# Kernel optimization log

Measured on AMD Instinct MI355X. Metric: run time of the kernel, lower is better.

Reference implementation:

```python
import jax, jax.numpy as jnp
import numpy as np

# Device / mapping constants (from iterator config in the original repo)
V_REF = 0.25
K_V = 2.0 * V_REF
G_MIN = 1e-5
G_MAX = 1e-3
N_AVG = 2.99
N_STD = 0.37
N_IN, N_OUT, BATCH = 1024, 512, 128


def setup_inputs() -> dict:
    key = jax.random.key(0)
    ks = jax.random.split(key, 6)
    x = jax.random.uniform(ks[0], (BATCH, N_IN), dtype=jnp.float32)
    stdv = 1.0 / np.sqrt(N_IN)
    w_pos = 0.5 + stdv * jax.random.normal(ks[1], (N_IN, N_OUT), dtype=jnp.float32)
    w_neg = 0.5 + stdv * jax.random.normal(ks[2], (N_IN, N_OUT), dtype=jnp.float32)
    b_pos = 0.5 * jnp.ones((N_OUT,), jnp.float32)
    b_neg = 0.5 * jnp.ones((N_OUT,), jnp.float32)
    # per-crosspoint I-V nonlinearity parameter n (n=2 means ohmic); clip below at 2
    n_devices = jnp.maximum(
        N_AVG + N_STD * jax.random.normal(ks[3], (N_IN + 1, 2 * N_OUT), dtype=jnp.float32),
        2.0,
    )
    return {"x": x, "w_pos": w_pos, "w_neg": w_neg, "b_pos": b_pos,
            "b_neg": b_neg, "n_devices": n_devices}


def reference(x, w_pos, w_neg, b_pos, b_neg, n_devices):
    B = x.shape[0]
    # append bias input of 1s -> [B, n_in+1]
    inputs = jnp.concatenate([x, jnp.ones((B, 1), x.dtype)], axis=1)
    # combined weights with bias row -> [n_in+1, n_out] each
    cw_pos = jnp.concatenate([w_pos, b_pos[None, :]], axis=0)
    cw_neg = jnp.concatenate([w_neg, b_neg[None, :]], axis=0)
    # interleave pos/neg columns -> [n_in+1, 2*n_out]
    combined = jnp.stack([cw_pos, cw_neg], axis=-1).reshape(cw_pos.shape[0], -1)
    # x -> V mapping
    V = K_V * inputs  # [B, n_in+1]
    # weight params -> conductances
    max_weight = jnp.max(jnp.abs(combined))
    k_G = (G_MAX - G_MIN) / max_weight
    G = k_G * jnp.abs(combined) + G_MIN  # [n_in+1, 2*n_out]
    # nonlinear I-V: I(V) = sign(V) * G*V_ref * (|V|/V_ref)^log2(n)
    exponent = jnp.log2(n_devices)          # [n_in+1, 2*n_out]
    sgn = jnp.sign(V)                       # [B, n_in+1]
    ratio = jnp.abs(V) / V_REF              # [B, n_in+1]
    I_ind = (sgn[:, :, None] * (G * V_REF)[None, :, :]
             * ratio[:, :, None] ** exponent[None, :, :])  # [B, n_in+1, 2*n_out]
    I = jnp.sum(I_ind, axis=1)              # [B, 2*n_out] (sum along bit lines)
    # differential pair currents -> output
    I_total = I[:, 0::2] - I[:, 1::2]       # [B, n_out]
    y = I_total / (K_V * k_G)
    return y
```

## Files before the change

kernel.cpp:

```cpp
#include <hip/hip_runtime.h>
#include <cstdint>
#include <cstddef>


#define B128 128
#define NIN  1024
#define NI   1025
#define NO   512
#define NJ   1024
#define SPLITS 32
#define CHUNK  33
#define GMIN 1.0e-5f
#define GSPAN (1.0e-3f - 1.0e-5f)

__device__ __forceinline__ float flog2(float x) { return __builtin_amdgcn_logf(x); }
__device__ __forceinline__ float fexp2(float x) { return __builtin_amdgcn_exp2f(x); }

__global__ __launch_bounds__(1024) void k_prep(
    const float* __restrict__ x,
    const float* __restrict__ wp, const float* __restrict__ wn,
    const float* __restrict__ bp, const float* __restrict__ bn,
    float* __restrict__ LT, float* __restrict__ bmax, float* __restrict__ out)
{
    const int tid = blockIdx.x * 1024 + threadIdx.x;

    if (tid < B128 * NO) out[tid] = 0.0f;

    if (tid < NI * B128) {
        int i = tid >> 7, b = tid & 127;
        float xv = (i < NIN) ? x[b * NIN + i] : 1.0f;
        LT[tid] = 1.0f + flog2(xv);
    }

    float m = fmaxf(fmaxf(__builtin_fabsf(wp[tid]), __builtin_fabsf(wn[tid])),
                    fmaxf(__builtin_fabsf(wp[tid + 262144]), __builtin_fabsf(wn[tid + 262144])));
    if (tid < NO) m = fmaxf(m, fmaxf(__builtin_fabsf(bp[tid]), __builtin_fabsf(bn[tid])));

    __shared__ float red[16];
    #pragma unroll
    for (int off = 32; off > 0; off >>= 1) m = fmaxf(m, __shfl_down(m, off, 64));
    if ((threadIdx.x & 63) == 0) red[threadIdx.x >> 6] = m;
    __syncthreads();
    if (threadIdx.x < 16) {
        m = red[threadIdx.x];
        #pragma unroll
        for (int off = 8; off > 0; off >>= 1) m = fmaxf(m, __shfl_down(m, off, 16));
        if (threadIdx.x == 0) bmax[blockIdx.x] = m;
    }
}

__global__ __launch_bounds__(1024, 4) void k_main(
    const float* __restrict__ nd,
    const float* __restrict__ wp, const float* __restrict__ wn,
    const float* __restrict__ bp, const float* __restrict__ bn,
    const float* __restrict__ LT, const float* __restrict__ bmax,
    float* __restrict__ out)
{
    const int lane = threadIdx.x & 63;

    float m = fmaxf(fmaxf(bmax[lane], bmax[lane + 64]),
                    fmaxf(bmax[lane + 128], bmax[lane + 192]));
    #pragma unroll
    for (int off = 32; off > 0; off >>= 1) m = fmaxf(m, __shfl_down(m, off, 64));
    const float maxw = __shfl(m, 0, 64);
    const float kG = GSPAN / maxw;
    const float C  = 0.5f * maxw / GSPAN;

    const int wvid = threadIdx.x >> 6;
    const int b0 = __builtin_amdgcn_readfirstlane(wvid << 3);
    const int o = (blockIdx.x << 6) + lane;
    const int i0 = blockIdx.y * CHUNK;
    int i1 = i0 + CHUNK; if (i1 > NI) i1 = NI;

    float2 acc[8];
    #pragma unroll
    for (int k = 0; k < 8; ++k) acc[k] = make_float2(0.0f, 0.0f);

    float2 nv = *(const float2*)(nd + (size_t)i0 * NJ + 2 * o);
    float wvp = (i0 < NIN) ? wp[i0 * NO + o] : bp[o];
    float wvn = (i0 < NIN) ? wn[i0 * NO + o] : bn[o];
    float4 L03 = *(const float4*)(LT + i0 * B128 + b0);
    float4 L47 = *(const float4*)(LT + i0 * B128 + b0 + 4);

    for (int i = i0; i < i1; ++i) {
        const int ip = (i + 1 < i1) ? i + 1 : i;
        float2 nv_n = *(const float2*)(nd + (size_t)ip * NJ + 2 * o);
        float wp_n = (ip < NIN) ? wp[ip * NO + o] : bp[o];
        float wn_n = (ip < NIN) ? wn[ip * NO + o] : bn[o];
        float4 L03n = *(const float4*)(LT + ip * B128 + b0);
        float4 L47n = *(const float4*)(LT + ip * B128 + b0 + 4);

        const float Ep = flog2(nv.x);
        const float En = flog2(nv.y);
        const float Wp = flog2(__builtin_fmaf(kG, __builtin_fabsf(wvp), GMIN));
        const float Wn = flog2(__builtin_fmaf(kG, __builtin_fabsf(wvn), GMIN));

        float Lv[8] = {L03.x, L03.y, L03.z, L03.w, L47.x, L47.y, L47.z, L47.w};
        #pragma unroll
        for (int bb = 0; bb < 8; ++bb) {
            const float L = Lv[bb];
            acc[bb].x += fexp2(__builtin_fmaf(Ep, L, Wp));
            acc[bb].y += fexp2(__builtin_fmaf(En, L, Wn));
        }

        nv = nv_n; wvp = wp_n; wvn = wn_n; L03 = L03n; L47 = L47n;
    }

    #pragma unroll
    for (int bb = 0; bb < 8; ++bb) {
        unsafeAtomicAdd(out + (size_t)(b0 + bb) * NO + o, C * (acc[bb].x - acc[bb].y));
    }
}

extern "C" void kernel_launch(void* const* d_in, const int* in_sizes, int n_in,
                              void* d_out, int out_size, void* d_ws, size_t ws_size,
                              hipStream_t stream)
{
    const float* x  = (const float*)d_in[0];
    const float* wp = (const float*)d_in[1];
    const float* wn = (const float*)d_in[2];
    const float* bp = (const float*)d_in[3];
    const float* bn = (const float*)d_in[4];
    const float* nd = (const float*)d_in[5];
    float* out = (float*)d_out;

    unsigned char* ws = (unsigned char*)d_ws;
    float* bmax = (float*)ws;
    float* LT   = (float*)(ws + 4096);

    k_prep<<<256, 1024, 0, stream>>>(x, wp, wn, bp, bn, LT, bmax, out);
    k_main<<<dim3(8, SPLITS), 1024, 0, stream>>>(nd, wp, wn, bp, bn, LT, bmax, out);
}
```

Before: 96.86 us.

## Precompute per-crosspoint log2 exponent and conductance in separate kernel

Adds a k_ew kernel that computes log2(n) and log2(G) for every crosspoint once and stores them as a float4 table. The main kernel then reads this table instead of recomputing four log2 per crosspoint in each of the 16 waves that share an output column. This removes redundant transcendental work, at the cost of an extra kernel launch and writing then reading an 8 MB intermediate table.

```diff
diff --git a/kernel.cpp b/kernel.cpp
--- a/kernel.cpp
+++ b/kernel.cpp
@@ -49,12 +49,43 @@
     }
 }
 
-__global__ __launch_bounds__(1024, 4) void k_main(
+__global__ __launch_bounds__(256) void k_ew(
     const float* __restrict__ nd,
     const float* __restrict__ wp, const float* __restrict__ wn,
     const float* __restrict__ bp, const float* __restrict__ bn,
-    const float* __restrict__ LT, const float* __restrict__ bmax,
-    float* __restrict__ out)
+    const float* __restrict__ bmax, float4* __restrict__ EWT)
+{
+    __shared__ float smax;
+    float m = bmax[threadIdx.x];
+    #pragma unroll
+    for (int off = 32; off > 0; off >>= 1) m = fmaxf(m, __shfl_down(m, off, 64));
+    __shared__ float red[4];
+    if ((threadIdx.x & 63) == 0) red[threadIdx.x >> 6] = m;
+    __syncthreads();
+    if (threadIdx.x == 0)
+        smax = fmaxf(fmaxf(red[0], red[1]), fmaxf(red[2], red[3]));
+    __syncthreads();
+    const float kG = GSPAN / smax;
+
+    const int tid = blockIdx.x * 256 + threadIdx.x;
+    if (tid >= NI * NO) return;
+    const int i = tid / NO, o = tid - i * NO;
+
+    const float2 nv = *(const float2*)(nd + (size_t)i * NJ + 2 * o);
+    const float wvp = (i < NIN) ? wp[i * NO + o] : bp[o];
+    const float wvn = (i < NIN) ? wn[i * NO + o] : bn[o];
+
+    float4 r;
+    r.x = flog2(nv.x);
+    r.y = flog2(__builtin_fmaf(kG, __builtin_fabsf(wvp), GMIN));
+    r.z = flog2(nv.y);
+    r.w = flog2(__builtin_fmaf(kG, __builtin_fabsf(wvn), GMIN));
+    EWT[tid] = r;
+}
+
+__global__ __launch_bounds__(1024, 4) void k_main(
+    const float4* __restrict__ EWT, const float* __restrict__ LT,
+    const float* __restrict__ bmax, float* __restrict__ out)
 {
     const int lane = threadIdx.x & 63;
 
@@ -63,52 +94,41 @@
     #pragma unroll
     for (int off = 32; off > 0; off >>= 1) m = fmaxf(m, __shfl_down(m, off, 64));
     const float maxw = __shfl(m, 0, 64);
-    const float kG = GSPAN / maxw;
     const float C  = 0.5f * maxw / GSPAN;
 
     const int wvid = threadIdx.x >> 6;
-    const int b0 = __builtin_amdgcn_readfirstlane(wvid << 3);
+    const int b0 = wvid << 3;
     const int o = (blockIdx.x << 6) + lane;
     const int i0 = blockIdx.y * CHUNK;
     int i1 = i0 + CHUNK; if (i1 > NI) i1 = NI;
 
-    float2 acc[8];
+    float accp[8], accn[8];
     #pragma unroll
-    for (int k = 0; k < 8; ++k) acc[k] = make_float2(0.0f, 0.0f);
+    for (int k = 0; k < 8; ++k) { accp[k] = 0.0f; accn[k] = 0.0f; }
 
-    float2 nv = *(const float2*)(nd + (size_t)i0 * NJ + 2 * o);
-    float wvp = (i0 < NIN) ? wp[i0 * NO + o] : bp[o];
-    float wvn = (i0 < NIN) ? wn[i0 * NO + o] : bn[o];
+    float4 ew  = EWT[(size_t)i0 * NO + o];
     float4 L03 = *(const float4*)(LT + i0 * B128 + b0);
     float4 L47 = *(const float4*)(LT + i0 * B128 + b0 + 4);
 
     for (int i = i0; i < i1; ++i) {
         const int ip = (i + 1 < i1) ? i + 1 : i;
-        float2 nv_n = *(const float2*)(nd + (size_t)ip * NJ + 2 * o);
-        float wp_n = (ip < NIN) ? wp[ip * NO + o] : bp[o];
-        float wn_n = (ip < NIN) ? wn[ip * NO + o] : bn[o];
+        float4 ew_n  = EWT[(size_t)ip * NO + o];
         float4 L03n = *(const float4*)(LT + ip * B128 + b0);
         float4 L47n = *(const float4*)(LT + ip * B128 + b0 + 4);
 
-        const float Ep = flog2(nv.x);
-        const float En = flog2(nv.y);
-        const float Wp = flog2(__builtin_fmaf(kG, __builtin_fabsf(wvp), GMIN));
-        const float Wn = flog2(__builtin_fmaf(kG, __builtin_fabsf(wvn), GMIN));
-
-        float Lv[8] = {L03.x, L03.y, L03.z, L03.w, L47.x, L47.y, L47.z, L47.w};
+        const float Lv[8] = {L03.x, L03.y, L03.z, L03.w, L47.x, L47.y, L47.z, L47.w};
         #pragma unroll
         for (int bb = 0; bb < 8; ++bb) {
-            const float L = Lv[bb];
-            acc[bb].x += fexp2(__builtin_fmaf(Ep, L, Wp));
-            acc[bb].y += fexp2(__builtin_fmaf(En, L, Wn));
+            accp[bb] += fexp2(__builtin_fmaf(ew.x, Lv[bb], ew.y));
+            accn[bb] += fexp2(__builtin_fmaf(ew.z, Lv[bb], ew.w));
         }
 
-        nv = nv_n; wvp = wp_n; wvn = wn_n; L03 = L03n; L47 = L47n;
+        ew = ew_n; L03 = L03n; L47 = L47n;
     }
 
     #pragma unroll
     for (int bb = 0; bb < 8; ++bb) {
-        unsafeAtomicAdd(out + (size_t)(b0 + bb) * NO + o, C * (acc[bb].x - acc[bb].y));
+        unsafeAtomicAdd(out + (size_t)(b0 + bb) * NO + o, C * (accp[bb] - accn[bb]));
     }
 }
 
@@ -127,7 +147,9 @@
     unsigned char* ws = (unsigned char*)d_ws;
     float* bmax = (float*)ws;
     float* LT   = (float*)(ws + 4096);
+    float4* EWT = (float4*)(ws + 4096 + 525056);
 
     k_prep<<<256, 1024, 0, stream>>>(x, wp, wn, bp, bn, LT, bmax, out);
-    k_main<<<dim3(8, SPLITS), 1024, 0, stream>>>(nd, wp, wn, bp, bn, LT, bmax, out);
+    k_ew<<<2050, 256, 0, stream>>>(nd, wp, wn, bp, bn, bmax, EWT);
+    k_main<<<dim3(8, SPLITS), 1024, 0, stream>>>(EWT, LT, bmax, out);
 }
```

Measured after the change: 100.9 us. 1.04x slower.

## Replace atomic split-K accumulation with per-block LDS reduction over inputs

Applied to the files above, without the earlier changes.

Work is repartitioned so that each block covers every input row for 64 outputs and 4 batch rows. Its 8 waves stride over the input dimension and their partial sums are reduced through shared memory, then written directly. This drops the global atomics and the zeroing of the output in the prep kernel. In exchange, the per-row log2 terms and the n_devices/weight loads are now repeated for twice as many batch groups, since each thread handles 4 batch rows instead of 8. Each thread also runs a much longer serial loop with half as many threads launched.

```diff
diff --git a/kernel.cpp b/kernel.cpp
--- a/kernel.cpp
+++ b/kernel.cpp
@@ -8,8 +8,6 @@
 #define NI   1025
 #define NO   512
 #define NJ   1024
-#define SPLITS 32
-#define CHUNK  33
 #define GMIN 1.0e-5f
 #define GSPAN (1.0e-3f - 1.0e-5f)
 
@@ -20,11 +18,9 @@
     const float* __restrict__ x,
     const float* __restrict__ wp, const float* __restrict__ wn,
     const float* __restrict__ bp, const float* __restrict__ bn,
-    float* __restrict__ LT, float* __restrict__ bmax, float* __restrict__ out)
+    float* __restrict__ LT, float* __restrict__ bmax)
 {
     const int tid = blockIdx.x * 1024 + threadIdx.x;
-
-    if (tid < B128 * NO) out[tid] = 0.0f;
 
     if (tid < NI * B128) {
         int i = tid >> 7, b = tid & 127;
@@ -49,7 +45,7 @@
     }
 }
 
-__global__ __launch_bounds__(1024, 4) void k_main(
+__global__ __launch_bounds__(512) void k_fused(
     const float* __restrict__ nd,
     const float* __restrict__ wp, const float* __restrict__ wn,
     const float* __restrict__ bp, const float* __restrict__ bn,
@@ -57,6 +53,9 @@
     float* __restrict__ out)
 {
     const int lane = threadIdx.x & 63;
+    const int s    = threadIdx.x >> 6;
+    const int o    = (blockIdx.x << 6) + lane;
+    const int b0   = blockIdx.y << 2;
 
     float m = fmaxf(fmaxf(bmax[lane], bmax[lane + 64]),
                     fmaxf(bmax[lane + 128], bmax[lane + 192]));
@@ -66,49 +65,57 @@
     const float kG = GSPAN / maxw;
     const float C  = 0.5f * maxw / GSPAN;
 
-    const int wvid = threadIdx.x >> 6;
-    const int b0 = __builtin_amdgcn_readfirstlane(wvid << 3);
-    const int o = (blockIdx.x << 6) + lane;
-    const int i0 = blockIdx.y * CHUNK;
-    int i1 = i0 + CHUNK; if (i1 > NI) i1 = NI;
+    float accp[4] = {0.f, 0.f, 0.f, 0.f};
+    float accn[4] = {0.f, 0.f, 0.f, 0.f};
 
-    float2 acc[8];
-    #pragma unroll
-    for (int k = 0; k < 8; ++k) acc[k] = make_float2(0.0f, 0.0f);
+    int i = s;
+    float2 nv = *(const float2*)(nd + (size_t)i * NJ + 2 * o);
+    float wvp = (i < NIN) ? wp[i * NO + o] : bp[o];
+    float wvn = (i < NIN) ? wn[i * NO + o] : bn[o];
+    float4 L4 = *(const float4*)(LT + i * B128 + b0);
 
-    float2 nv = *(const float2*)(nd + (size_t)i0 * NJ + 2 * o);
-    float wvp = (i0 < NIN) ? wp[i0 * NO + o] : bp[o];
-    float wvn = (i0 < NIN) ? wn[i0 * NO + o] : bn[o];
-    float4 L03 = *(const float4*)(LT + i0 * B128 + b0);
-    float4 L47 = *(const float4*)(LT + i0 * B128 + b0 + 4);
-
-    for (int i = i0; i < i1; ++i) {
-        const int ip = (i + 1 < i1) ? i + 1 : i;
+    while (i < NI) {
+        const int ip = (i + 8 < NI) ? i + 8 : i;
         float2 nv_n = *(const float2*)(nd + (size_t)ip * NJ + 2 * o);
         float wp_n = (ip < NIN) ? wp[ip * NO + o] : bp[o];
         float wn_n = (ip < NIN) ? wn[ip * NO + o] : bn[o];
-        float4 L03n = *(const float4*)(LT + ip * B128 + b0);
-        float4 L47n = *(const float4*)(LT + ip * B128 + b0 + 4);
+        float4 L4n = *(const float4*)(LT + ip * B128 + b0);
 
         const float Ep = flog2(nv.x);
         const float En = flog2(nv.y);
         const float Wp = flog2(__builtin_fmaf(kG, __builtin_fabsf(wvp), GMIN));
         const float Wn = flog2(__builtin_fmaf(kG, __builtin_fabsf(wvn), GMIN));
 
-        float Lv[8] = {L03.x, L03.y, L03.z, L03.w, L47.x, L47.y, L47.z, L47.w};
+        const float Lv[4] = {L4.x, L4.y, L4.z, L4.w};
         #pragma unroll
-        for (int bb = 0; bb < 8; ++bb) {
-            const float L = Lv[bb];
-            acc[bb].x += fexp2(__builtin_fmaf(Ep, L, Wp));
-            acc[bb].y += fexp2(__builtin_fmaf(En, L, Wn));
+        for (int j = 0; j < 4; ++j) {
+            accp[j] += fexp2(__builtin_fmaf(Ep, Lv[j], Wp));
+            accn[j] += fexp2(__builtin_fmaf(En, Lv[j], Wn));
         }
 
-        nv = nv_n; wvp = wp_n; wvn = wn_n; L03 = L03n; L47 = L47n;
+        nv = nv_n; wvp = wp_n; wvn = wn_n; L4 = L4n;
+        i += 8;
     }
 
-    #pragma unroll
-    for (int bb = 0; bb < 8; ++bb) {
-        unsafeAtomicAdd(out + (size_t)(b0 + bb) * NO + o, C * (acc[bb].x - acc[bb].y));
+    __shared__ float lds[8 * 64 * 9];
+    {
+        const int base = (s * 64 + lane) * 9;
+        #pragma unroll
+        for (int j = 0; j < 4; ++j) { lds[base + j] = accp[j]; lds[base + 4 + j] = accn[j]; }
+    }
+    __syncthreads();
+
+    if (threadIdx.x < 256) {
+        const int l = threadIdx.x & 63;
+        const int b = threadIdx.x >> 6;
+        float sp = 0.f, sn = 0.f;
+        #pragma unroll
+        for (int w = 0; w < 8; ++w) {
+            const int base = (w * 64 + l) * 9;
+            sp += lds[base + b];
+            sn += lds[base + 4 + b];
+        }
+        out[(size_t)(b0 + b) * NO + (blockIdx.x << 6) + l] = C * (sp - sn);
     }
 }
 
@@ -128,6 +135,6 @@
     float* bmax = (float*)ws;
     float* LT   = (float*)(ws + 4096);
 
-    k_prep<<<256, 1024, 0, stream>>>(x, wp, wn, bp, bn, LT, bmax, out);
-    k_main<<<dim3(8, SPLITS), 1024, 0, stream>>>(nd, wp, wn, bp, bn, LT, bmax, out);
+    k_prep<<<256, 1024, 0, stream>>>(x, wp, wn, bp, bn, LT, bmax);
+    k_fused<<<dim3(8, 32), 512, 0, stream>>>(nd, wp, wn, bp, bn, LT, bmax, out);
 }
```

Result: slower. 123.2 us (+27.2%).
